# Kernel tuning notes

Hardware: AMD Instinct MI355X
Metric: run time of the kernel (lower is better)

## Reference

```python
import jax, jax.numpy as jnp
import numpy as np
import math

N = 8192       # number of cells (spatial tokens)
D = 512        # d_model
H = 512        # attn_hidden_dim (defaults to d_model)
GAMMA = 0.5    # real/fake mixing weight


def setup_inputs() -> dict:
    key = jax.random.key(0)
    ks = jax.random.split(key, 9)
    s = 1.0 / math.sqrt(D)  # nn.Linear-like init scale -> stable exp(scores)
    x = jax.random.normal(ks[0], (N, D), dtype=jnp.float32)
    real_edge_mask = jax.random.bernoulli(ks[1], 0.5, (N, N))
    fake_edge_mask = jax.random.bernoulli(ks[2], 0.5, (N, N))
    Wq_real = jax.random.normal(ks[3], (D, H), dtype=jnp.float32) * s
    Wk_real = jax.random.normal(ks[4], (D, H), dtype=jnp.float32) * s
    Wq_fake = jax.random.normal(ks[5], (D, H), dtype=jnp.float32) * s
    Wk_fake = jax.random.normal(ks[6], (D, H), dtype=jnp.float32) * s
    Wv = jax.random.normal(ks[7], (D, D), dtype=jnp.float32) * s
    bv = jnp.zeros((D,), dtype=jnp.float32)
    return dict(x=x, real_edge_mask=real_edge_mask, fake_edge_mask=fake_edge_mask,
                Wq_real=Wq_real, Wk_real=Wk_real, Wq_fake=Wq_fake, Wk_fake=Wk_fake,
                Wv=Wv, bv=bv)


def reference(x, real_edge_mask, fake_edge_mask, Wq_real, Wk_real, Wq_fake, Wk_fake, Wv, bv):
    scale = 1.0 / math.sqrt(H)
    neg = jnp.float32(-1e9)
    # real branch scores [N, N]
    sr = jnp.einsum('nh,mh->nm', x @ Wq_real, x @ Wk_real) * scale
    sr = jnp.where(real_edge_mask, neg, sr)
    # fake branch scores [N, N]
    sf = jnp.einsum('nh,mh->nm', x @ Wq_fake, x @ Wk_fake) * scale
    sf = jnp.where(fake_edge_mask, neg, sf)
    # NOTE: original computes row maxima but never uses them (dead code);
    # it exponentiates raw scores directly -- replicated faithfully.
    scores = (jnp.exp(sr) + GAMMA * jnp.exp(sf)) / (1.0 + GAMMA)
    attn = scores / jnp.sum(scores, axis=-1, keepdims=True)
    V = x @ Wv + bv
    cntx = attn @ V
    return cntx, attn
```

## Files before the change

kernel.cpp:

```cpp
#include <hip/hip_runtime.h>


#define K_N 8192
#define K_D 512

typedef float  f32x4 __attribute__((ext_vector_type(4)));
typedef _Float16 f16x8 __attribute__((ext_vector_type(8)));
typedef unsigned short u16;
typedef unsigned int u32;

__device__ __forceinline__ u16 f2h(float f) {
  _Float16 h = (_Float16)f;
  return __builtin_bit_cast(u16, h);
}
__device__ __forceinline__ float h2f(u16 b) {
  return (float)__builtin_bit_cast(_Float16, b);
}

__device__ __forceinline__ void gload_lds16(const void* g, void* l) {
  __builtin_amdgcn_global_load_lds(
      (const __attribute__((address_space(1))) void*)g,
      (__attribute__((address_space(3))) void*)l, 16, 0, 0);
}

__device__ __forceinline__ void nt_store4(float* p, f32x4 v) {
  __builtin_nontemporal_store(v, (f32x4*)p);
}

__global__ void k_detect(const unsigned char* __restrict__ m, int* __restrict__ flag) {
  __shared__ int any;
  if (threadIdx.x == 0) any = 0;
  __syncthreads();
  int local = 0;
  for (int i = threadIdx.x; i < 65536; i += 256)
    local |= m[4 * i + 1];
  if (local) atomicOr(&any, 1);
  __syncthreads();
  if (threadIdx.x == 0) *flag = any ? 1 : 0;
}

__device__ __forceinline__ bool mask_at(const void* mask, int mode, size_t idx) {
  if (mode) return ((const unsigned char*)mask)[idx] != 0;
  return ((const int*)mask)[idx] != 0;
}

__device__ __forceinline__ u32 pack_word(const void* m, int mode, int r, int c) {
  u32 out = 0;
  if (mode) {
    const uint4* p = (const uint4*)((const unsigned char*)m + (size_t)r * K_N + c * 32);
    uint4 a = p[0], b = p[1];
    u32 ws[8] = {a.x, a.y, a.z, a.w, b.x, b.y, b.z, b.w};
#pragma unroll
    for (int i = 0; i < 8; i++) {
      u32 v = ws[i];
      v |= v >> 4; v |= v >> 2; v |= v >> 1;
      v &= 0x01010101u;
      out |= (v & 1u) << (4 * i);
      out |= ((v >> 8) & 1u) << (4 * i + 1);
      out |= ((v >> 16) & 1u) << (4 * i + 2);
      out |= ((v >> 24) & 1u) << (4 * i + 3);
    }
  } else {
    const uint4* p = (const uint4*)((const int*)m + (size_t)r * K_N + c * 32);
#pragma unroll
    for (int i = 0; i < 8; i++) {
      uint4 v = p[i];
      out |= (v.x ? 1u : 0u) << (4 * i);
      out |= (v.y ? 1u : 0u) << (4 * i + 1);
      out |= (v.z ? 1u : 0u) << (4 * i + 2);
      out |= (v.w ? 1u : 0u) << (4 * i + 3);
    }
  }
  return out;
}

__global__ __launch_bounds__(256) void k_packmask2(
    const void* __restrict__ mR, const void* __restrict__ mF,
    const int* __restrict__ flag,
    u32* __restrict__ bR, u32* __restrict__ bF) {
  __shared__ u32 sm[32][129];
  const int mode = *flag;
  const int tid = threadIdx.x;
  const int r0 = blockIdx.x * 128;
  const int c0 = blockIdx.y * 32;

#pragma unroll
  for (int t = 0; t < 2; ++t) {
    const void* m = t ? mF : mR;
    u32* dst = t ? bF : bR;
    if (t) __syncthreads();
#pragma unroll 4
    for (int i = 0; i < 16; ++i) {
      int idx = i * 256 + tid;
      int r = idx >> 5, c = idx & 31;
      sm[c][r] = pack_word(m, mode, r0 + r, c0 + c);
    }
    __syncthreads();
#pragma unroll 4
    for (int i = 0; i < 16; ++i) {
      int idx = i * 256 + tid;
      int c = idx >> 7, r = idx & 127;
      dst[(size_t)(c0 + c) * K_N + r0 + r] = sm[c][r];
    }
  }
}

__global__ void k_cvt_x(const float* __restrict__ x, u16* __restrict__ xh) {
  int i = blockIdx.x * 256 + threadIdx.x;
  float4 v = ((const float4*)x)[i];
  ushort4 o;
  o.x = f2h(v.x); o.y = f2h(v.y); o.z = f2h(v.z); o.w = f2h(v.w);
  ((ushort4*)xh)[i] = o;
}

__global__ void k_zero(float* __restrict__ p) {
  size_t i = (size_t)blockIdx.x * 256 + threadIdx.x;
  ((float4*)p)[i] = make_float4(0.f, 0.f, 0.f, 0.f);
}

template <int IN_F32>
__global__ void k_transpose(const void* __restrict__ in, u16* __restrict__ out,
                            int R, int C) {
  __shared__ u16 sm[64][65];
  int c0 = blockIdx.x * 64, r0 = blockIdx.y * 64;
#pragma unroll
  for (int e = 0; e < 16; e++) {
    int idx = e * 256 + threadIdx.x;
    int i = idx >> 6, j = idx & 63;
    u16 h;
    if (IN_F32) h = f2h(((const float*)in)[(size_t)(r0 + i) * C + c0 + j]);
    else        h = ((const u16*)in)[(size_t)(r0 + i) * C + c0 + j];
    sm[i][j] = h;
  }
  __syncthreads();
#pragma unroll
  for (int e = 0; e < 16; e++) {
    int idx = e * 256 + threadIdx.x;
    int j = idx >> 6, i = idx & 63;
    out[(size_t)(c0 + j) * R + r0 + i] = sm[i][j];
  }
}

template <int A_F32>
__device__ __forceinline__ void gemm_core(const void* __restrict__ Ap, int lda,
                                          const u16* __restrict__ Bt, int ldb,
                                          int rowBase, int colBase, int K,
                                          u16* sA, u16* sB, f32x4 (&acc)[4][4]) {
  const int tid   = threadIdx.x;
  const int lane  = tid & 63;
  const int waveM = tid >> 7;
  const int waveN = (tid >> 6) & 1;
  const int lrow  = lane & 15;
  const int lk    = lane >> 4;

  for (int k0 = 0; k0 < K; k0 += 64) {
    __syncthreads();
#pragma unroll
    for (int g = 0; g < 4; g++) {
      int cid = g * 256 + tid;
      int row = cid >> 3;
      int pk  = cid & 7;
      int k16 = pk ^ (row & 7);
      if (A_F32) {
        const float* s = (const float*)Ap + (size_t)(rowBase + row) * lda + k0 + k16 * 8;
        float4 v0 = *(const float4*)s;
        float4 v1 = *(const float4*)(s + 4);
        ushort4 h0, h1;
        h0.x = f2h(v0.x); h0.y = f2h(v0.y); h0.z = f2h(v0.z); h0.w = f2h(v0.w);
        h1.x = f2h(v1.x); h1.y = f2h(v1.y); h1.z = f2h(v1.z); h1.w = f2h(v1.w);
        *(ushort4*)&sA[cid * 8]     = h0;
        *(ushort4*)&sA[cid * 8 + 4] = h1;
      } else {
        uint4 v = *(const uint4*)((const u16*)Ap + (size_t)(rowBase + row) * lda + k0 + k16 * 8);
        *(uint4*)&sA[cid * 8] = v;
      }
      uint4 w = *(const uint4*)(Bt + (size_t)(colBase + row) * ldb + k0 + k16 * 8);
      *(uint4*)&sB[cid * 8] = w;
    }
    __syncthreads();
#pragma unroll
    for (int kk = 0; kk < 2; kk++) {
      f16x8 af[4], bfv[4];
      int k16 = kk * 4 + lk;
#pragma unroll
      for (int mb = 0; mb < 4; mb++) {
        int r = waveM * 64 + mb * 16 + lrow;
        af[mb] = *(const f16x8*)&sA[r * 64 + ((k16 ^ (r & 7)) << 3)];
      }
#pragma unroll
      for (int nb = 0; nb < 4; nb++) {
        int c = waveN * 64 + nb * 16 + lrow;
        bfv[nb] = *(const f16x8*)&sB[c * 64 + ((k16 ^ (c & 7)) << 3)];
      }
#pragma unroll
      for (int mb = 0; mb < 4; mb++)
#pragma unroll
        for (int nb = 0; nb < 4; nb++)
          acc[mb][nb] = __builtin_amdgcn_mfma_f32_16x16x32_f16(af[mb], bfv[nb], acc[mb][nb], 0, 0, 0);
    }
  }
}

__global__ __launch_bounds__(256) void k_proj(const u16* __restrict__ xh,
                                              const u16* __restrict__ wt,
                                              u16* __restrict__ qr, u16* __restrict__ kr,
                                              u16* __restrict__ qf, u16* __restrict__ kf,
                                              u16* __restrict__ vh,
                                              const float* __restrict__ bv) {
  __shared__ u16 sA[128 * 64], sB[128 * 64];
  f32x4 acc[4][4] = {};
  const int z = blockIdx.z;
  const int rowBase = blockIdx.y * 128, colBase = blockIdx.x * 128;
  gemm_core<0>(xh, K_D, wt + (size_t)z * 262144, K_D, rowBase, colBase, K_D, sA, sB, acc);

  u16* out = (z == 0) ? qr : (z == 1) ? kr : (z == 2) ? qf : (z == 3) ? kf : vh;
  const int lane = threadIdx.x & 63;
  const int waveM = threadIdx.x >> 7, waveN = (threadIdx.x >> 6) & 1;
  const int lrow = lane & 15, lk = lane >> 4;
#pragma unroll
  for (int mb = 0; mb < 4; mb++)
#pragma unroll
    for (int nb = 0; nb < 4; nb++)
#pragma unroll
      for (int r = 0; r < 4; r++) {
        int grow = rowBase + waveM * 64 + mb * 16 + lk * 4 + r;
        int gcol = colBase + waveN * 64 + nb * 16 + lrow;
        float v = acc[mb][nb][r];
        if (z == 4) v += bv[gcol];
        out[(size_t)grow * K_D + gcol] = f2h(v);
      }
}

__global__ __launch_bounds__(256, 2) void k_scores2(
    const u16* __restrict__ qr, const u16* __restrict__ kr,
    const u16* __restrict__ qf, const u16* __restrict__ kf,
    const u32* __restrict__ bitR, const u32* __restrict__ bitF,
    u16* __restrict__ outp, float* __restrict__ partial) {

  __shared__ u16 s[2][2][8192];

  const int tid = threadIdx.x;
  const int lane = tid & 63, wid = tid >> 6;

  int b = blockIdx.x + (blockIdx.y << 6);
  int xcd = b & 7, j = b >> 3;
  const int by = xcd * 8 + (j & 7);
  const int bx = j >> 3;
  const int rowBase = by * 128, colBase = bx * 128;

  const u16* qrB = qr + (size_t)rowBase * K_D;
  const u16* krB = kr + (size_t)colBase * K_D;
  const u16* qfB = qf + (size_t)rowBase * K_D;
  const u16* kfB = kf + (size_t)colBase * K_D;

  f32x4 accR[4][4] = {}, accF[4][4] = {};

  auto STAGE = [&](int buf, const u16* qb, const u16* kb, int k0) {
#pragma unroll
    for (int jj = 0; jj < 4; ++jj) {
      int cid = jj * 256 + tid;
      int row = cid >> 3;
      int k16 = (cid & 7) ^ (row & 7);
      gload_lds16(qb + (size_t)row * K_D + k0 + k16 * 8,
                  &s[buf][0][(jj * 256 + wid * 64) * 8]);
      gload_lds16(kb + (size_t)row * K_D + k0 + k16 * 8,
                  &s[buf][1][(jj * 256 + wid * 64) * 8]);
    }
  };

  const int waveM = wid >> 1;
  const int waveN = wid & 1;
  const int lrow = lane & 15, lk = lane >> 4;

  auto COMPUTE = [&](f32x4 (&acc)[4][4], int cur) {
#pragma unroll
    for (int kk = 0; kk < 2; ++kk) {
      int k16 = kk * 4 + lk;
      f16x8 a[4], bb[4];
#pragma unroll
      for (int mb = 0; mb < 4; ++mb) {
        int r = waveM * 64 + mb * 16 + lrow;
        a[mb] = *(const f16x8*)&s[cur][0][r * 64 + ((k16 ^ (r & 7)) << 3)];
      }
#pragma unroll
      for (int nb = 0; nb < 4; ++nb) {
        int c = waveN * 64 + nb * 16 + lrow;
        bb[nb] = *(const f16x8*)&s[cur][1][c * 64 + ((k16 ^ (c & 7)) << 3)];
      }
#pragma unroll
      for (int mb = 0; mb < 4; ++mb)
#pragma unroll
        for (int nb = 0; nb < 4; ++nb)
          acc[mb][nb] = __builtin_amdgcn_mfma_f32_16x16x32_f16(a[mb], bb[nb], acc[mb][nb], 0, 0, 0);
    }
  };

  STAGE(0, qrB, krB, 0);
  __syncthreads();
  int cur = 0;
  for (int it = 0; it < 8; ++it) {
    if (it < 7) STAGE(cur ^ 1, qrB, krB, (it + 1) * 64);
    else        STAGE(cur ^ 1, qfB, kfB, 0);
    COMPUTE(accR, cur);
    __syncthreads();
    cur ^= 1;
  }
  for (int it = 0; it < 8; ++it) {
    if (it < 7) STAGE(cur ^ 1, qfB, kfB, (it + 1) * 64);
    COMPUTE(accF, cur);
    __syncthreads();
    cur ^= 1;
  }

  const float scale = 0.04419417382415922f;
  u16* vt16 = (u16*)&s[0][0][0];

#pragma unroll
  for (int mb = 0; mb < 4; ++mb)
#pragma unroll
    for (int rr = 0; rr < 4; ++rr) {
      int growl = waveM * 64 + mb * 16 + lk * 4 + rr;
      int grow = rowBase + growl;
      u32 wR0 = bitR[(size_t)(bx * 4 + waveN * 2 + 0) * K_N + grow];
      u32 wR1 = bitR[(size_t)(bx * 4 + waveN * 2 + 1) * K_N + grow];
      u32 wF0 = bitF[(size_t)(bx * 4 + waveN * 2 + 0) * K_N + grow];
      u32 wF1 = bitF[(size_t)(bx * 4 + waveN * 2 + 1) * K_N + grow];
      float rs = 0.f;
#pragma unroll
      for (int nb = 0; nb < 4; ++nb) {
        int cc = nb * 16 + lrow;
        int gcoll = waveN * 64 + cc;
        u32 wR = (cc >> 5) ? wR1 : wR0;
        u32 wF = (cc >> 5) ? wF1 : wF0;
        int bitpos = cc & 31;
        bool m1 = (wR >> bitpos) & 1u;
        bool m2 = (wF >> bitpos) & 1u;
        float er = m1 ? 0.f : __expf(accR[mb][nb][rr] * scale);
        float ef = m2 ? 0.f : __expf(accF[mb][nb][rr] * scale);
        float v = er + 0.5f * ef;
        rs += v;
        vt16[growl * 136 + gcoll] = f2h(v);
      }
      rs += __shfl_xor(rs, 1, 64);
      rs += __shfl_xor(rs, 2, 64);
      rs += __shfl_xor(rs, 4, 64);
      rs += __shfl_xor(rs, 8, 64);
      if (lrow == 0)
        partial[(size_t)grow * 128 + bx * 2 + waveN] = rs;
    }
  __syncthreads();

#pragma unroll
  for (int jj = 0; jj < 8; ++jj) {
    int f = jj * 256 + tid;
    int row = f >> 4, seg = f & 15;
    uint4 v = *(const uint4*)&vt16[row * 136 + seg * 8];
    *(uint4*)&outp[(size_t)(rowBase + row) * K_N + colBase + seg * 8] = v;
  }
}

template <int F16OUT, int USEBITS>
__global__ __launch_bounds__(512, 2) void k_scores8(
    const u16* __restrict__ qr, const u16* __restrict__ kr,
    const u16* __restrict__ qf, const u16* __restrict__ kf,
    const u32* __restrict__ bitR, const u32* __restrict__ bitF,
    const void* __restrict__ mR, const void* __restrict__ mF,
    const int* __restrict__ flag,
    void* __restrict__ outp, float* __restrict__ partial) {

  __shared__ u16 s[2][4][8192];

  const int tid = threadIdx.x;
  const int lane = tid & 63, wid = tid >> 6;
  const int bx = blockIdx.x, by = blockIdx.y;
  const int rowBase = by * 128, colBase = bx * 128;

  const u16* base0 = qr + (size_t)rowBase * K_D;
  const u16* base1 = kr + (size_t)colBase * K_D;
  const u16* base2 = qf + (size_t)rowBase * K_D;
  const u16* base3 = kf + (size_t)colBase * K_D;

  f32x4 accR[4][2] = {}, accF[4][2] = {};

  auto STAGE = [&](int b, int k0) {
    const u16* bases[4] = {base0, base1, base2, base3};
#pragma unroll
    for (int t = 0; t < 4; ++t)
#pragma unroll
      for (int j = 0; j < 2; ++j) {
        int cid = j * 512 + tid;
        int row = cid >> 3;
        int k16 = (cid & 7) ^ (row & 7);
        gload_lds16(bases[t] + (size_t)row * K_D + k0 + k16 * 8,
                    &s[b][t][(j * 512 + wid * 64) * 8]);
      }
  };

  STAGE(0, 0);
  __syncthreads();

  const int waveM = wid >> 2, waveN = wid & 3;
  const int lrow = lane & 15, lk = lane >> 4;

  int cur = 0;
  for (int it = 0; it < 8; ++it) {
    if (it < 7) STAGE(cur ^ 1, (it + 1) * 64);
#pragma unroll
    for (int kk = 0; kk < 2; ++kk) {
      int k16 = kk * 4 + lk;
      f16x8 aR[4], aF[4], bR[2], bF[2];
#pragma unroll
      for (int mb = 0; mb < 4; ++mb) {
        int r = waveM * 64 + mb * 16 + lrow;
        int off = r * 64 + ((k16 ^ (r & 7)) << 3);
        aR[mb] = *(const f16x8*)&s[cur][0][off];
        aF[mb] = *(const f16x8*)&s[cur][2][off];
      }
#pragma unroll
      for (int nb = 0; nb < 2; ++nb) {
        int c = waveN * 32 + nb * 16 + lrow;
        int off = c * 64 + ((k16 ^ (c & 7)) << 3);
        bR[nb] = *(const f16x8*)&s[cur][1][off];
        bF[nb] = *(const f16x8*)&s[cur][3][off];
      }
#pragma unroll
      for (int mb = 0; mb < 4; ++mb)
#pragma unroll
        for (int nb = 0; nb < 2; ++nb) {
          accR[mb][nb] = __builtin_amdgcn_mfma_f32_16x16x32_f16(aR[mb], bR[nb], accR[mb][nb], 0, 0, 0);
          accF[mb][nb] = __builtin_amdgcn_mfma_f32_16x16x32_f16(aF[mb], bF[nb], accF[mb][nb], 0, 0, 0);
        }
    }
    __syncthreads();
    cur ^= 1;
  }

  const float scale = 0.04419417382415922f;
  const int mode = USEBITS ? 0 : *flag;
  u16*   vt16 = (u16*)&s[0][0][0];
  float* vt32 = (float*)&s[0][0][0];

#pragma unroll
  for (int mb = 0; mb < 4; ++mb)
#pragma unroll
    for (int rr = 0; rr < 4; ++rr) {
      int growl = waveM * 64 + mb * 16 + lk * 4 + rr;
      int grow = rowBase + growl;
      u32 wR = 0, wF = 0;
      if (USEBITS) {
        wR = bitR[(size_t)(bx * 4 + waveN) * K_N + grow];
        wF = bitF[(size_t)(bx * 4 + waveN) * K_N + grow];
      }
      float rs = 0.f;
#pragma unroll
      for (int nb = 0; nb < 2; ++nb) {
        int bitpos = nb * 16 + lrow;
        int gcoll = waveN * 32 + bitpos;
        bool m1, m2;
        if (USEBITS) {
          m1 = (wR >> bitpos) & 1u;
          m2 = (wF >> bitpos) & 1u;
        } else {
          size_t oi = (size_t)grow * K_N + colBase + gcoll;
          m1 = mask_at(mR, mode, oi);
          m2 = mask_at(mF, mode, oi);
        }
        float er = m1 ? 0.f : __expf(accR[mb][nb][rr] * scale);
        float ef = m2 ? 0.f : __expf(accF[mb][nb][rr] * scale);
        float v = er + 0.5f * ef;
        rs += v;
        if (F16OUT) vt16[growl * 136 + gcoll] = f2h(v);
        else        vt32[growl * 132 + gcoll] = v;
      }
      rs += __shfl_xor(rs, 1, 64);
      rs += __shfl_xor(rs, 2, 64);
      rs += __shfl_xor(rs, 4, 64);
      rs += __shfl_xor(rs, 8, 64);
      if (lrow == 0)
        partial[(size_t)grow * 256 + bx * 4 + waveN] = rs;
    }
  __syncthreads();

  if (F16OUT) {
    u16* out = (u16*)outp;
#pragma unroll
    for (int j = 0; j < 4; ++j) {
      int f = j * 512 + tid;
      int row = f >> 4, seg = f & 15;
      uint4 v = *(const uint4*)&vt16[row * 136 + seg * 8];
      *(uint4*)&out[(size_t)(rowBase + row) * K_N + colBase + seg * 8] = v;
    }
  } else {
    float* out = (float*)outp;
#pragma unroll
    for (int j = 0; j < 8; ++j) {
      int f = j * 512 + tid;
      int row = f >> 5, seg = f & 31;
      float4 v = *(const float4*)&vt32[row * 132 + seg * 4];
      *(float4*)&out[(size_t)(rowBase + row) * K_N + colBase + seg * 4] = v;
    }
  }
}

template <int STRIDE>
__global__ void k_rowsum(const float* __restrict__ partial, float* __restrict__ inv) {
  int r = blockIdx.x * 256 + threadIdx.x;
  const float4* p = (const float4*)(partial + (size_t)r * STRIDE);
  float s = 0.f;
#pragma unroll 8
  for (int j = 0; j < STRIDE / 4; j++) {
    float4 v = p[j];
    s += v.x + v.y + v.z + v.w;
  }
  inv[r] = 1.0f / s;
}

__global__ void k_norm_b(float* __restrict__ attn, const float* __restrict__ inv) {
  const size_t total = (size_t)K_N * K_N / 4;
  for (size_t i = (size_t)blockIdx.x * 256 + threadIdx.x; i < total;
       i += (size_t)gridDim.x * 256) {
    int row = (int)(i >> 11);
    float s = inv[row];
    float4 v = ((float4*)attn)[i];
    v.x *= s; v.y *= s; v.z *= s; v.w *= s;
    ((float4*)attn)[i] = v;
  }
}

__global__ __launch_bounds__(256, 4) void k_cntx6(
    const u16* __restrict__ sh, const u16* __restrict__ vT,
    const float* __restrict__ inv, float* __restrict__ cntx,
    float* __restrict__ attn) {
  __shared__ u16 sA[128 * 64], sB[128 * 64];
  f32x4 acc[4][4] = {};

  const int tid = threadIdx.x;
  int b = blockIdx.x + (blockIdx.y << 3);
  int xcd = b & 7, j = b >> 3;
  const int s  = xcd + 8 * (j >> 4);
  const int u  = j & 15;
  const int ch = u >> 2;
  const int ks = u & 3;
  const int rowBase = s * 128, colBase = ch * 128;
  const int k0 = ks * 2048;

  gemm_core<0>(sh + (size_t)k0, K_N, vT + (size_t)k0, K_N,
               rowBase, colBase, 2048, sA, sB, acc);

  const int lane = tid & 63;
  const int waveM = tid >> 7, waveN = (tid >> 6) & 1;
  const int lrow = lane & 15, lk = lane >> 4;
#pragma unroll
  for (int mb = 0; mb < 4; mb++)
#pragma unroll
    for (int rr = 0; rr < 4; rr++) {
      int grow = rowBase + waveM * 64 + mb * 16 + lk * 4 + rr;
      float iv = inv[grow];
#pragma unroll
      for (int nb = 0; nb < 4; nb++) {
        int gcol = colBase + waveN * 64 + nb * 16 + lrow;
        atomicAdd(&cntx[(size_t)grow * K_D + gcol], acc[mb][nb][rr] * iv);
      }
    }

  const int ac0 = ks * 2048 + ch * 512;
  const u16* src = sh + (size_t)rowBase * K_N + ac0;
  float* ad = attn + (size_t)rowBase * K_N + ac0;
  for (int i = tid; i < 128 * 64; i += 256) {
    int row = i >> 6, c8 = i & 63;
    float sc = inv[rowBase + row];
    uint4 v = *(const uint4*)&src[(size_t)row * K_N + c8 * 8];
    f32x4 o0, o1;
    o0.x = h2f(v.x & 0xFFFF) * sc; o0.y = h2f(v.x >> 16) * sc;
    o0.z = h2f(v.y & 0xFFFF) * sc; o0.w = h2f(v.y >> 16) * sc;
    o1.x = h2f(v.z & 0xFFFF) * sc; o1.y = h2f(v.z >> 16) * sc;
    o1.z = h2f(v.w & 0xFFFF) * sc; o1.w = h2f(v.w >> 16) * sc;
    float* d2 = ad + (size_t)row * K_N + c8 * 8;
    nt_store4(d2, o0);
    nt_store4(d2 + 4, o1);
  }
}

template <int A_F32>
__global__ __launch_bounds__(256) void k_cntx(const void* __restrict__ Ap,
                                              const u16* __restrict__ vT,
                                              const float* __restrict__ inv,
                                              float* __restrict__ out) {
  __shared__ u16 sA[128 * 64], sB[128 * 64];
  f32x4 acc[4][4] = {};
  int b = blockIdx.x + blockIdx.y * 4;
  int c = b & 7, jj = b >> 3;
  int xb = jj & 3, yb = c + 8 * (jj >> 2);
  const int rowBase = yb * 128, colBase = xb * 128;
  gemm_core<A_F32>(Ap, K_N, vT, K_N, rowBase, colBase, K_N, sA, sB, acc);

  const int lane = threadIdx.x & 63;
  const int waveM = threadIdx.x >> 7, waveN = (threadIdx.x >> 6) & 1;
  const int lrow = lane & 15, lk = lane >> 4;
#pragma unroll
  for (int mb = 0; mb < 4; mb++)
#pragma unroll
    for (int r = 0; r < 4; r++) {
      int grow = rowBase + waveM * 64 + mb * 16 + lk * 4 + r;
      float iv = inv[grow];
#pragma unroll
      for (int nb = 0; nb < 4; nb++) {
        int gcol = colBase + waveN * 64 + nb * 16 + lrow;
        out[(size_t)grow * K_D + gcol] = acc[mb][nb][r] * iv;
      }
    }
}

extern "C" void kernel_launch(void* const* d_in, const int* in_sizes, int n_in,
                              void* d_out, int out_size, void* d_ws, size_t ws_size,
                              hipStream_t stream) {
  const float* x   = (const float*)d_in[0];
  const void*  mR  = d_in[1];
  const void*  mF  = d_in[2];
  const float* Wv  = (const float*)d_in[7];
  const float* bv  = (const float*)d_in[8];

  const size_t ND = (size_t)K_N * K_D;
  u16* xh = (u16*)d_ws;
  u16* qr = xh + ND;
  u16* kr = qr + ND;
  u16* qf = kr + ND;
  u16* kf = qf + ND;
  u16* vh = kf + ND;
  u16* vT = vh + ND;
  u16* wt = vT + ND;
  u32* bitR = (u32*)(wt + 5 * 262144);
  u32* bitF = bitR + (size_t)K_N * 256;
  u16* sh   = (u16*)(bitF + (size_t)K_N * 256);

  const size_t need_bits = (size_t)((char*)sh - (char*)d_ws) + 64;
  const size_t need_sh   = (size_t)((char*)sh - (char*)d_ws) + (size_t)K_N * K_N * 2;
  const bool have_bits = ws_size >= need_bits;
  const bool have_sh   = ws_size >= need_sh;

  float* cntx = (float*)d_out;
  float* attn = cntx + ND;
  float* partial = (float*)d_ws;
  float* inv     = (float*)qr;
  int* flag = have_bits ? (int*)sh : (int*)cntx;

  k_detect<<<1, 256, 0, stream>>>((const unsigned char*)mR, flag);
  if (have_bits)
    k_packmask2<<<dim3(64, 8), 256, 0, stream>>>(mR, mF, flag, bitR, bitF);

  k_cvt_x<<<4096, 256, 0, stream>>>(x, xh);
  k_transpose<1><<<dim3(8, 8), 256, 0, stream>>>((const void*)d_in[3], wt + 0 * 262144, 512, 512);
  k_transpose<1><<<dim3(8, 8), 256, 0, stream>>>((const void*)d_in[4], wt + 1 * 262144, 512, 512);
  k_transpose<1><<<dim3(8, 8), 256, 0, stream>>>((const void*)d_in[5], wt + 2 * 262144, 512, 512);
  k_transpose<1><<<dim3(8, 8), 256, 0, stream>>>((const void*)d_in[6], wt + 3 * 262144, 512, 512);
  k_transpose<1><<<dim3(8, 8), 256, 0, stream>>>(Wv,  wt + 4 * 262144, 512, 512);

  k_proj<<<dim3(4, 64, 5), 256, 0, stream>>>(xh, wt, qr, kr, qf, kf, vh, bv);
  k_transpose<0><<<dim3(8, 128), 256, 0, stream>>>(vh, vT, K_N, K_D);

  if (have_sh && have_bits) {
    k_scores2<<<dim3(64, 64), 256, 0, stream>>>(qr, kr, qf, kf, bitR, bitF, sh, partial);
    k_rowsum<128><<<32, 256, 0, stream>>>(partial, inv);
    k_zero<<<4096, 256, 0, stream>>>(cntx);
    k_cntx6<<<dim3(8, 128), 256, 0, stream>>>(sh, vT, inv, cntx, attn);
  } else if (have_bits) {
    k_scores8<0, 1><<<dim3(64, 64), 512, 0, stream>>>(qr, kr, qf, kf, bitR, bitF,
                                                      mR, mF, flag, attn, partial);
    k_rowsum<256><<<32, 256, 0, stream>>>(partial, inv);
    k_cntx<1><<<dim3(4, 64), 256, 0, stream>>>(attn, vT, inv, cntx);
    k_norm_b<<<8192, 256, 0, stream>>>(attn, inv);
  } else {
    k_scores8<0, 0><<<dim3(64, 64), 512, 0, stream>>>(qr, kr, qf, kf, nullptr, nullptr,
                                                      mR, mF, flag, attn, partial);
    k_rowsum<256><<<32, 256, 0, stream>>>(partial, inv);
    k_cntx<1><<<dim3(4, 64), 256, 0, stream>>>(attn, vT, inv, cntx);
    k_norm_b<<<8192, 256, 0, stream>>>(attn, inv);
  }
}
```

Measured before the change: 580.8 us.

## Drop LDS double buffering in score kernel to raise occupancy to 4 blocks

```diff
diff --git a/kernel.cpp b/kernel.cpp
--- a/kernel.cpp
+++ b/kernel.cpp
@@ -231,13 +231,15 @@
       }
 }
 
-__global__ __launch_bounds__(256, 2) void k_scores2(
+__global__ __launch_bounds__(256, 4) void k_scores2(
     const u16* __restrict__ qr, const u16* __restrict__ kr,
     const u16* __restrict__ qf, const u16* __restrict__ kf,
     const u32* __restrict__ bitR, const u32* __restrict__ bitF,
     u16* __restrict__ outp, float* __restrict__ partial) {
 
-  __shared__ u16 s[2][2][8192];
+  __shared__ u16 smem[17408];
+  u16* sQ = smem;
+  u16* sK = smem + 8192;
 
   const int tid = threadIdx.x;
   const int lane = tid & 63, wid = tid >> 6;
@@ -255,16 +257,16 @@
 
   f32x4 accR[4][4] = {}, accF[4][4] = {};
 
-  auto STAGE = [&](int buf, const u16* qb, const u16* kb, int k0) {
+  auto STAGE = [&](const u16* qb, const u16* kb, int k0) {
 #pragma unroll
     for (int jj = 0; jj < 4; ++jj) {
       int cid = jj * 256 + tid;
       int row = cid >> 3;
       int k16 = (cid & 7) ^ (row & 7);
       gload_lds16(qb + (size_t)row * K_D + k0 + k16 * 8,
-                  &s[buf][0][(jj * 256 + wid * 64) * 8]);
+                  &sQ[(jj * 256 + wid * 64) * 8]);
       gload_lds16(kb + (size_t)row * K_D + k0 + k16 * 8,
-                  &s[buf][1][(jj * 256 + wid * 64) * 8]);
+                  &sK[(jj * 256 + wid * 64) * 8]);
     }
   };
 
@@ -272,7 +274,7 @@
   const int waveN = wid & 1;
   const int lrow = lane & 15, lk = lane >> 4;
 
-  auto COMPUTE = [&](f32x4 (&acc)[4][4], int cur) {
+  auto COMPUTE = [&](f32x4 (&acc)[4][4]) {
 #pragma unroll
     for (int kk = 0; kk < 2; ++kk) {
       int k16 = kk * 4 + lk;
@@ -280,12 +282,12 @@
 #pragma unroll
       for (int mb = 0; mb < 4; ++mb) {
         int r = waveM * 64 + mb * 16 + lrow;
-        a[mb] = *(const f16x8*)&s[cur][0][r * 64 + ((k16 ^ (r & 7)) << 3)];
+        a[mb] = *(const f16x8*)&sQ[r * 64 + ((k16 ^ (r & 7)) << 3)];
       }
 #pragma unroll
       for (int nb = 0; nb < 4; ++nb) {
         int c = waveN * 64 + nb * 16 + lrow;
-        bb[nb] = *(const f16x8*)&s[cur][1][c * 64 + ((k16 ^ (c & 7)) << 3)];
+        bb[nb] = *(const f16x8*)&sK[c * 64 + ((k16 ^ (c & 7)) << 3)];
       }
 #pragma unroll
       for (int mb = 0; mb < 4; ++mb)
@@ -295,25 +297,18 @@
     }
   };
 
-  STAGE(0, qrB, krB, 0);
+  for (int t = 0; t < 16; ++t) {
+    __syncthreads();
+    if (t < 8) STAGE(qrB, krB, t * 64);
+    else       STAGE(qfB, kfB, (t - 8) * 64);
+    __syncthreads();
+    if (t < 8) COMPUTE(accR);
+    else       COMPUTE(accF);
+  }
   __syncthreads();
-  int cur = 0;
-  for (int it = 0; it < 8; ++it) {
-    if (it < 7) STAGE(cur ^ 1, qrB, krB, (it + 1) * 64);
-    else        STAGE(cur ^ 1, qfB, kfB, 0);
-    COMPUTE(accR, cur);
-    __syncthreads();
-    cur ^= 1;
-  }
-  for (int it = 0; it < 8; ++it) {
-    if (it < 7) STAGE(cur ^ 1, qfB, kfB, (it + 1) * 64);
-    COMPUTE(accF, cur);
-    __syncthreads();
-    cur ^= 1;
-  }
 
   const float scale = 0.04419417382415922f;
-  u16* vt16 = (u16*)&s[0][0][0];
+  u16* vt16 = smem;
 
 #pragma unroll
   for (int mb = 0; mb < 4; ++mb)
```

Measured after the change: 2.208 ms. 3.8x slower.
